# Kernel optimization log

Hardware: AMD Instinct MI355X
Metric: run time of the kernel (lower is better)

Reference implementation:

```python
import jax, jax.numpy as jnp
import numpy as np

N = 197          # tokens (== token_count)
B = 64           # batch
D = 768          # d_model
NH = 12          # n_head
GH = 2           # global_heads
HR = NH // GH    # head_ratio = 6
DH = 64          # d_head
QK = GH * DH     # qk_dim = 128
ML = 3           # mask_levels
EPS = 1e-5


def setup_inputs() -> dict:
    key = jax.random.key(0)
    ks = jax.random.split(key, 9)
    s = 1.0 / np.sqrt(D)
    return {
        "h": jax.random.normal(ks[0], (N, B, D), dtype=jnp.float32),
        "masks": jax.random.uniform(ks[1], (N, N, ML), dtype=jnp.float32),
        "Wq": jax.random.normal(ks[2], (QK, D), dtype=jnp.float32) * s,
        "Wk": jax.random.normal(ks[3], (QK, D), dtype=jnp.float32) * s,
        "Wv": jax.random.normal(ks[4], (NH * DH, D), dtype=jnp.float32) * s,
        "Wo": jax.random.normal(ks[5], (D, NH * DH), dtype=jnp.float32) * s,
        "mask_proj": jnp.ones((ML, NH), dtype=jnp.float32),
        "ln_gamma": jnp.ones((D,), dtype=jnp.float32),
        "ln_beta": jnp.zeros((D,), dtype=jnp.float32),
    }


def reference(h, masks, Wq, Wk, Wv, Wo, mask_proj, ln_gamma, ln_beta):
    scale = 1.0 / np.sqrt(DH)
    # projections (seq-first layout [N, B, ...])
    q = (h @ Wq.T).reshape(N, B, GH, DH)
    k = (h @ Wk.T).reshape(N, B, GH, DH)
    v = (h @ Wv.T).reshape(N, B, NH, DH)
    # global-head scores: [B, GH, i, j]
    score = jnp.einsum('ibgd,jbgd->bgij', q, k) * scale
    # learned mask mix: [i, j, NH] -> [GH, i, j, HR] (g-major head split, matches torch reshape)
    mw = jnp.einsum('ijl,ln->ijn', masks, mask_proj)
    mw = mw.reshape(N, N, GH, HR).transpose(2, 0, 1, 3)
    # broadcast each global head to HR local heads: [B, GH, i, j, HR]
    attn = score[..., None] * mw[None]
    attn = attn.transpose(0, 1, 4, 2, 3).reshape(B, NH, N, N)  # head = g*HR + r
    prob = jax.nn.softmax(attn, axis=-1)
    # AV: [i, B, NH, DH] -> [N, B, NH*DH]
    vec = jnp.einsum('bnij,jbnd->ibnd', prob, v).reshape(N, B, NH * DH)
    out = vec @ Wo.T
    # post-LN residual
    x = h + out
    mu = jnp.mean(x, axis=-1, keepdims=True)
    var = jnp.var(x, axis=-1, keepdims=True)
    return ln_gamma * (x - mu) / jnp.sqrt(var + EPS) + ln_beta
```

## Files before the change

### kernel.cpp

```cpp
#include <hip/hip_runtime.h>
#include <hip/hip_bf16.h>
#include <stdint.h>

#define NTOK 197
#define NPAD 224
#define BATCH 64
#define DMODEL 768
#define NHEAD 12
#define GHEAD 2
#define HRATIO 6
#define DHEAD 64
#define QKDIM 128
#define LNEPS 1e-5f
#define MROWS (NTOK * BATCH)
#define MPAD 12672
#define NKC 24
#define NBAND 99

using f32x4 = __attribute__((ext_vector_type(4))) float;
using s16x8 = __attribute__((ext_vector_type(8))) short;
using s16x4 = __attribute__((ext_vector_type(4))) short;

__device__ __forceinline__ short f2bf(float f) {
  unsigned int x = __float_as_uint(f);
  return (short)((x + 0x7fffu + ((x >> 16) & 1u)) >> 16);
}

__device__ __forceinline__ float bf2f(short s) {
  return __uint_as_float((unsigned)(unsigned short)s << 16);
}

__device__ __forceinline__ void gld16(void* lds, const void* g) {
  __builtin_amdgcn_global_load_lds(
      (const __attribute__((address_space(1))) unsigned int*)g,
      (__attribute__((address_space(3))) unsigned int*)lds, 16, 0, 0);
}

#define NBH (NBAND * NKC)
#define NBQ (8 * NKC)
#define NBW (6 * NKC)
__global__ __launch_bounds__(256)
void prep_kernel(const float* __restrict__ h, const float* __restrict__ Wq,
                 const float* __restrict__ Wk, const float* __restrict__ Wv,
                 const float* __restrict__ Wo, short* __restrict__ hf,
                 short* __restrict__ Wqkvf, short* __restrict__ Wof) {
  const int bb = blockIdx.x, t = threadIdx.x;
  int band, kc, which;
  if (bb < NBH) { which = 0; band = bb / NKC; kc = bb - band * NKC; }
  else if (bb < NBH + NBQ) { int i = bb - NBH; which = 1; band = i / NKC; kc = i - band * NKC; }
  else { int i = bb - NBH - NBQ; which = 2; band = i / NKC; kc = i - band * NKC; }
  short* dstS = (which == 0 ? hf : which == 1 ? Wqkvf : Wof) +
                ((size_t)(band * NKC + kc) * 8) * 512;
#pragma unroll
  for (int uu = 0; uu < 2; ++uu) {
    int u = t + uu * 256;
    int frag = u >> 6, l = u & 63;
    int rl = frag * 16 + (l & 15);
    int k0 = kc * 32 + ((l >> 4) & 3) * 8;
    float4 a = {0, 0, 0, 0}, c = {0, 0, 0, 0};
    if (which == 0) {
      int row = band * 128 + rl;
      if (row < MROWS) {
        const float* p = h + (size_t)row * DMODEL + k0;
        a = *(const float4*)p; c = *(const float4*)(p + 4);
      }
    } else if (which == 1) {
      int row = band * 128 + rl;
      const float* src = (row < 128) ? Wq + (size_t)row * DMODEL
                       : (row < 256) ? Wk + (size_t)(row - 128) * DMODEL
                                     : Wv + (size_t)(row - 256) * DMODEL;
      a = *(const float4*)(src + k0); c = *(const float4*)(src + k0 + 4);
    } else {
      const float* p = Wo + (size_t)(band * 128 + rl) * DMODEL + k0;
      a = *(const float4*)p; c = *(const float4*)(p + 4);
    }
    s16x8 o;
    o[0] = f2bf(a.x); o[1] = f2bf(a.y); o[2] = f2bf(a.z); o[3] = f2bf(a.w);
    o[4] = f2bf(c.x); o[5] = f2bf(c.y); o[6] = f2bf(c.z); o[7] = f2bf(c.w);
    *(s16x8*)(dstS + (size_t)u * 8) = o;
  }
}

__global__ __launch_bounds__(256)
void gemm_frag_kernel(const short* __restrict__ Af, const short* __restrict__ Bf,
                      short* __restrict__ Cout, int M, int NC) {
  const int tid = threadIdx.x;
  const int nwg = gridDim.x * gridDim.y;
  const int orig = blockIdx.y * gridDim.x + blockIdx.x;
  const int qq = nwg >> 3, rr = nwg & 7;
  const int xcd = orig & 7, sidx = orig >> 3;
  const int wg = (xcd < rr ? xcd * (qq + 1) : rr * (qq + 1) + (xcd - rr) * qq) + sidx;
  const int cb = wg % gridDim.x;
  const int rb = wg / gridDim.x;

  const int w = tid >> 6, l = tid & 63;
  const int wr = w >> 1, wc = w & 1;
  const int lm = l & 15, lh = l >> 4;

  const short* pa = Af + ((size_t)(rb * NKC) * 8 + wr * 4) * 512 + l * 8;
  const short* pb = Bf + ((size_t)(cb * NKC) * 8 + wc * 4) * 512 + l * 8;

  f32x4 acc[4][4] = {};
  s16x8 A0[4], B0[4], A1[4], B1[4];

#define LOADF(Ar, Br, kc)                                   \
  do {                                                      \
    const short* qa = pa + (size_t)(kc) * 4096;             \
    const short* qb = pb + (size_t)(kc) * 4096;             \
    Ar[0] = *(const s16x8*)(qa);                            \
    Ar[1] = *(const s16x8*)(qa + 512);                      \
    Ar[2] = *(const s16x8*)(qa + 1024);                     \
    Ar[3] = *(const s16x8*)(qa + 1536);                     \
    Br[0] = *(const s16x8*)(qb);                            \
    Br[1] = *(const s16x8*)(qb + 512);                      \
    Br[2] = *(const s16x8*)(qb + 1024);                     \
    Br[3] = *(const s16x8*)(qb + 1536);                     \
  } while (0)

#define MM(Ar, Br)                                                             \
  do {                                                                         \
    _Pragma("unroll") for (int m = 0; m < 4; ++m)                              \
      _Pragma("unroll") for (int n = 0; n < 4; ++n)                            \
        acc[m][n] = __builtin_amdgcn_mfma_f32_16x16x32_bf16(Ar[m], Br[n],      \
                                                            acc[m][n], 0, 0, 0);\
  } while (0)

  LOADF(A0, B0, 0);
#pragma unroll
  for (int kc = 0; kc < NKC; kc += 2) {
    LOADF(A1, B1, kc + 1);
    MM(A0, B0);
    if (kc + 2 < NKC) LOADF(A0, B0, kc + 2);
    MM(A1, B1);
  }
#undef LOADF
#undef MM

#pragma unroll
  for (int m = 0; m < 4; ++m) {
#pragma unroll
    for (int r = 0; r < 4; ++r) {
      int row = rb * 128 + wr * 64 + m * 16 + lh * 4 + r;
      if (row < M) {
#pragma unroll
        for (int n = 0; n < 4; ++n) {
          int col = cb * 128 + wc * 64 + n * 16 + lm;
          Cout[(size_t)row * NC + col] = f2bf(acc[m][n][r]);
        }
      }
    }
  }
}

__global__ __launch_bounds__(256)
void packall_kernel(const short* __restrict__ Cb, const float* __restrict__ masks,
                    const float* __restrict__ mproj, short* __restrict__ qp,
                    short* __restrict__ kp, short* __restrict__ vT,
                    float* __restrict__ mwp) {
  __shared__ short Vs[NPAD][DHEAD + 1];
  const int bb = blockIdx.x, t = threadIdx.x;
  if (bb < 256) {
    int b = bb >> 2, g = (bb >> 1) & 1, which = bb & 1;
    short* dst = (which ? kp : qp) + ((size_t)b * GHEAD + g) * NPAD * 64;
    int d = t & 63, iofs = t >> 6;
    for (int i0 = 0; i0 < NPAD; i0 += 4) {
      int i = i0 + iofs;
      short v = 0;
      if (i < NTOK)
        v = Cb[(size_t)(i * BATCH + b) * 1024 + which * QKDIM + g * DHEAD + d];
      int dd = which ? ((((d >> 3) ^ (i & 7)) << 3) | (d & 7)) : d;
      dst[i * 64 + dd] = v;
    }
  } else if (bb < 1024) {
    int vv = bb - 256;
    int b = vv / 12, n = vv - b * 12;
    int d = t & 63, iofs = t >> 6;
    for (int i0 = 0; i0 < NPAD; i0 += 4) {
      int i = i0 + iofs;
      short v = 0;
      if (i < NTOK)
        v = Cb[(size_t)(i * BATCH + b) * 1024 + 256 + n * DHEAD + d];
      Vs[i][d] = v;
    }
    __syncthreads();
    short* dst = vT + ((size_t)b * NHEAD + n) * DHEAD * NPAD;
    int sub = t & 63, dr = t >> 6;
    for (int d0 = 0; d0 < DHEAD; d0 += 4) {
      if (sub < 56) {
        int dd = d0 + dr, j0 = sub * 4;
        s16x4 o;
        o[0] = Vs[j0][dd]; o[1] = Vs[j0 + 1][dd];
        o[2] = Vs[j0 + 2][dd]; o[3] = Vs[j0 + 3][dd];
        *(s16x4*)(dst + dd * NPAD + j0) = o;
      }
    }
  } else {
    int e = (bb - 1024) * 256 + t;
    int n = e >> 12;
    int rem = e & 4095;
    int i = rem >> 4, lm = rem & 15;
    float p0 = mproj[n], p1 = mproj[NHEAD + n], p2 = mproj[2 * NHEAD + n];
    float vals[16];
#pragma unroll
    for (int jf = 0; jf < 16; ++jf) vals[jf] = 0.f;
    if (i < NTOK) {
#pragma unroll
      for (int jf = 0; jf < 14; ++jf) {
        int col = jf * 16 + lm;
        if (col < NTOK) {
          const float* mp = masks + ((size_t)i * NTOK + col) * 3;
          vals[jf] = 0.125f * (mp[0] * p0 + mp[1] * p1 + mp[2] * p2);
        }
      }
    }
    float* dst = mwp + (size_t)e * 16;
#pragma unroll
    for (int q = 0; q < 4; ++q) {
      float4 o = make_float4(vals[q * 4], vals[q * 4 + 1], vals[q * 4 + 2], vals[q * 4 + 3]);
      *(float4*)(dst + q * 4) = o;
    }
  }
}

__global__ __launch_bounds__(256, 2)
void attn_fused_kernel(const short* __restrict__ qp, const short* __restrict__ kp,
                       const short* __restrict__ vT, const float* __restrict__ mwp,
                       short* __restrict__ vec_f) {
  const int it = blockIdx.x, b = blockIdx.y, g = blockIdx.z;
  __shared__ short Ks[NPAD * 64];
  __shared__ short Pt[64 * 256];
  __shared__ float rsb[64];
  const int t = threadIdx.x, w = t >> 6, l = t & 63;
  const int lm = l & 15, lh = l >> 4, l7 = l & 7;

  const short* qg = qp + ((size_t)b * GHEAD + g) * NPAD * 64;
  const short* kg = kp + ((size_t)b * GHEAD + g) * NPAD * 64;

#pragma unroll
  for (int s = 0; s < 7; ++s)
    gld16(Ks + s * 2048 + t * 8, kg + s * 2048 + t * 8);
  int qrow = it * 64 + w * 16 + lm;
  if (qrow > NPAD - 1) qrow = NPAD - 1;
  s16x8 a0 = *(const s16x8*)(qg + qrow * 64 + lh * 8);
  s16x8 a1 = *(const s16x8*)(qg + qrow * 64 + 32 + lh * 8);
  __syncthreads();

  f32x4 acc[14] = {};
#pragma unroll
  for (int jf = 0; jf < 14; ++jf) {
    s16x8 kf0 = *(const s16x8*)((const char*)Ks + (jf * 16 + lm) * 128 + ((lh ^ l7) << 4));
    s16x8 kf1 = *(const s16x8*)((const char*)Ks + (jf * 16 + lm) * 128 + (((4 + lh) ^ l7) << 4));
    acc[jf] = __builtin_amdgcn_mfma_f32_16x16x32_bf16(a0, kf0, acc[jf], 0, 0, 0);
    acc[jf] = __builtin_amdgcn_mfma_f32_16x16x32_bf16(a1, kf1, acc[jf], 0, 0, 0);
  }

  const int b4 = b >> 4;
  const int lofs = ((((w & 1) << 1) + (lm >> 3)) * 16 + (b & 15)) * 8 + (lm & 7);

  for (int hh = 0; hh < HRATIO; ++hh) {
    const int n = g * HRATIO + hh;
    const short* vg = vT + ((size_t)b * NHEAD + n) * 64 * NPAD;
    s16x8 vf[7];
#pragma unroll
    for (int ks = 0; ks < 7; ++ks)
      vf[ks] = *(const s16x8*)(vg + (w * 16 + lm) * NPAD + ks * 32 + lh * 8);

#pragma unroll
    for (int r = 0; r < 4; ++r) {
      const int row = w * 16 + lh * 4 + r;
      const int i = it * 64 + row;
      const float* mr = mwp + (((size_t)n * 256 + i) * 16 + lm) * 16;
      f32x4 mv0 = *(const f32x4*)(mr);
      f32x4 mv1 = *(const f32x4*)(mr + 4);
      f32x4 mv2 = *(const f32x4*)(mr + 8);
      f32x4 mv3 = *(const f32x4*)(mr + 12);
      float sum = 0.f;
#pragma unroll
      for (int jf = 0; jf < 13; ++jf) {
        float mwv = (jf < 4) ? mv0[jf] : (jf < 8) ? mv1[jf - 4]
                  : (jf < 12) ? mv2[jf - 8] : mv3[jf - 12];
        float pe = __expf(acc[jf][r] * mwv);
        if (jf == 12 && lm >= 5) pe = 0.f;
        sum += pe;
        int byteoff = row * 512 + (((2 * jf + (lm >> 3)) ^ (row & 7)) << 4) + (lm & 7) * 2;
        *(short*)((char*)Pt + byteoff) = f2bf(pe);
      }
      {
        int byteoff = row * 512 + (((26 + (lm >> 3)) ^ (row & 7)) << 4) + (lm & 7) * 2;
        *(short*)((char*)Pt + byteoff) = 0;
      }
#pragma unroll
      for (int off = 8; off; off >>= 1) sum += __shfl_xor(sum, off);
      if (lm == 0) rsb[row] = 1.f / sum;
    }
    __syncthreads();

    __builtin_amdgcn_s_setprio(1);
    f32x4 oacc[4] = {};
#pragma unroll
    for (int fi = 0; fi < 4; ++fi)
#pragma unroll
      for (int ks = 0; ks < 7; ++ks) {
        s16x8 pa = *(const s16x8*)((const char*)Pt + (fi * 16 + lm) * 512 +
                                   (((ks * 4 + lh) ^ l7) << 4));
        oacc[fi] = __builtin_amdgcn_mfma_f32_16x16x32_bf16(pa, vf[ks], oacc[fi], 0, 0, 0);
      }
    __builtin_amdgcn_s_setprio(0);
    const int kcH = n * 2 + (w >> 1);
#pragma unroll
    for (int fi = 0; fi < 4; ++fi)
#pragma unroll
      for (int r = 0; r < 4; ++r) {
        int ia = it * 64 + fi * 16 + lh * 4 + r;
        if (ia < NTOK) {
          float rsv = rsb[fi * 16 + lh * 4 + r];
          int fragidx = ((it * 32 + fi * 8 + lh * 2 + (r >> 1)) * NKC + kcH) * 8 +
                        ((r & 1) << 2) + b4;
          vec_f[(size_t)fragidx * 512 + lofs] = f2bf(oacc[fi][r] * rsv);
        }
      }
    __syncthreads();
  }
}

__global__ __launch_bounds__(256)
void ln_kernel(const float* __restrict__ h, const short* __restrict__ proj_b,
               float* __restrict__ out, const float* __restrict__ gamma,
               const float* __restrict__ beta) {
  const int m = blockIdx.x;
  const float* hrow = h + (size_t)m * DMODEL;
  const short* prow = proj_b + (size_t)m * DMODEL;
  float* orow = out + (size_t)m * DMODEL;
  const int tid = threadIdx.x;
  float v0 = hrow[tid] + bf2f(prow[tid]);
  float v1 = hrow[tid + 256] + bf2f(prow[tid + 256]);
  float v2 = hrow[tid + 512] + bf2f(prow[tid + 512]);
  float s = v0 + v1 + v2;
  float sq = v0 * v0 + v1 * v1 + v2 * v2;
#pragma unroll
  for (int off = 32; off; off >>= 1) {
    s += __shfl_xor(s, off);
    sq += __shfl_xor(sq, off);
  }
  __shared__ float ss[4], ssq[4];
  const int w = tid >> 6, lane = tid & 63;
  if (lane == 0) { ss[w] = s; ssq[w] = sq; }
  __syncthreads();
  s = ss[0] + ss[1] + ss[2] + ss[3];
  sq = ssq[0] + ssq[1] + ssq[2] + ssq[3];
  const float inv = 1.0f / (float)DMODEL;
  float mu = s * inv;
  float var = sq * inv - mu * mu;
  float rstd = rsqrtf(var + LNEPS);
  orow[tid] = gamma[tid] * (v0 - mu) * rstd + beta[tid];
  orow[tid + 256] = gamma[tid + 256] * (v1 - mu) * rstd + beta[tid + 256];
  orow[tid + 512] = gamma[tid + 512] * (v2 - mu) * rstd + beta[tid + 512];
}

extern "C" void kernel_launch(void* const* d_in, const int* in_sizes, int n_in,
                              void* d_out, int out_size, void* d_ws, size_t ws_size,
                              hipStream_t stream) {
  const float* h     = (const float*)d_in[0];
  const float* masks = (const float*)d_in[1];
  const float* Wq    = (const float*)d_in[2];
  const float* Wk    = (const float*)d_in[3];
  const float* Wv    = (const float*)d_in[4];
  const float* Wo    = (const float*)d_in[5];
  const float* mproj = (const float*)d_in[6];
  const float* gamma = (const float*)d_in[7];
  const float* beta  = (const float*)d_in[8];
  float* out = (float*)d_out;

  char* ws = (char*)d_ws;
  size_t o = 0;
  auto alloc = [&](size_t bytes) { size_t r = o; o += (bytes + 255) & ~(size_t)255; return r; };
  short* hf    = (short*)(ws + alloc((size_t)MPAD * DMODEL * 2));
  short* Cb    = (short*)(ws + alloc((size_t)MPAD * 1024 * 2));
  short* Wqkvf = (short*)(ws + alloc((size_t)1024 * DMODEL * 2));
  short* Wof   = (short*)(ws + alloc((size_t)DMODEL * DMODEL * 2));
  short* qp    = (short*)(ws + alloc((size_t)BATCH * GHEAD * NPAD * DHEAD * 2));
  short* kp    = (short*)(ws + alloc((size_t)BATCH * GHEAD * NPAD * DHEAD * 2));
  short* vT    = (short*)(ws + alloc((size_t)BATCH * NHEAD * DHEAD * NPAD * 2));
  float* mwp   = (float*)(ws + alloc((size_t)NHEAD * 256 * 16 * 16 * 4));
  short* vec_f = hf;
  short* proj_b = Cb;

  prep_kernel<<<NBH + NBQ + NBW, 256, 0, stream>>>(h, Wq, Wk, Wv, Wo, hf, Wqkvf, Wof);
  gemm_frag_kernel<<<dim3(8, NBAND), 256, 0, stream>>>(hf, Wqkvf, Cb, MROWS, 1024);
  packall_kernel<<<1216, 256, 0, stream>>>(Cb, masks, mproj, qp, kp, vT, mwp);
  attn_fused_kernel<<<dim3(4, BATCH, GHEAD), 256, 0, stream>>>(qp, kp, vT, mwp, vec_f);
  gemm_frag_kernel<<<dim3(6, NBAND), 256, 0, stream>>>(vec_f, Wof, proj_b, MROWS, DMODEL);
  ln_kernel<<<MROWS, 256, 0, stream>>>(h, proj_b, out, gamma, beta);
}
```

Baseline: 144.1 us.

## Split attention heads across more blocks, share LDS, write row-major output

The attention kernel now launches 1024 blocks, each handling three of the six local heads, with an XCD-aware block index mapping. K and P tiles share a single LDS buffer so four blocks fit per CU. Attention output is written in plain row-major bf16 instead of the pre-swizzled fragment layout, and the output-projection GEMM gains a template mode that reads A fragments directly from row-major memory. This raises occupancy and parallelism in attention, but the QK^T product is now computed twice per (b, g, it), and the GEMM's A loads become strided.

```diff
diff --git a/kernel.cpp b/kernel.cpp
--- a/kernel.cpp
+++ b/kernel.cpp
@@ -81,6 +81,7 @@
   }
 }
 
+template<int AM>
 __global__ __launch_bounds__(256)
 void gemm_frag_kernel(const short* __restrict__ Af, const short* __restrict__ Bf,
                       short* __restrict__ Cout, int M, int NC) {
@@ -98,23 +99,32 @@
   const int lm = l & 15, lh = l >> 4;
 
   const short* pa = Af + ((size_t)(rb * NKC) * 8 + wr * 4) * 512 + l * 8;
+  const short* paR = Af + (size_t)(rb * 128 + wr * 64 + lm) * DMODEL + lh * 8;
   const short* pb = Bf + ((size_t)(cb * NKC) * 8 + wc * 4) * 512 + l * 8;
 
   f32x4 acc[4][4] = {};
   s16x8 A0[4], B0[4], A1[4], B1[4];
 
-#define LOADF(Ar, Br, kc)                                   \
-  do {                                                      \
-    const short* qa = pa + (size_t)(kc) * 4096;             \
-    const short* qb = pb + (size_t)(kc) * 4096;             \
-    Ar[0] = *(const s16x8*)(qa);                            \
-    Ar[1] = *(const s16x8*)(qa + 512);                      \
-    Ar[2] = *(const s16x8*)(qa + 1024);                     \
-    Ar[3] = *(const s16x8*)(qa + 1536);                     \
-    Br[0] = *(const s16x8*)(qb);                            \
-    Br[1] = *(const s16x8*)(qb + 512);                      \
-    Br[2] = *(const s16x8*)(qb + 1024);                     \
-    Br[3] = *(const s16x8*)(qb + 1536);                     \
+#define LOADF(Ar, Br, kc)                                       \
+  do {                                                          \
+    if (AM == 0) {                                              \
+      const short* qa = pa + (size_t)(kc) * 4096;               \
+      Ar[0] = *(const s16x8*)(qa);                              \
+      Ar[1] = *(const s16x8*)(qa + 512);                        \
+      Ar[2] = *(const s16x8*)(qa + 1024);                       \
+      Ar[3] = *(const s16x8*)(qa + 1536);                       \
+    } else {                                                    \
+      const short* qa = paR + (kc) * 32;                        \
+      Ar[0] = *(const s16x8*)(qa);                              \
+      Ar[1] = *(const s16x8*)(qa + 16 * DMODEL);                \
+      Ar[2] = *(const s16x8*)(qa + 32 * DMODEL);                \
+      Ar[3] = *(const s16x8*)(qa + 48 * DMODEL);                \
+    }                                                           \
+    const short* qb = pb + (size_t)(kc) * 4096;                 \
+    Br[0] = *(const s16x8*)(qb);                                \
+    Br[1] = *(const s16x8*)(qb + 512);                          \
+    Br[2] = *(const s16x8*)(qb + 1024);                         \
+    Br[3] = *(const s16x8*)(qb + 1536);                         \
   } while (0)
 
 #define MM(Ar, Br)                                                             \
@@ -222,13 +232,20 @@
   }
 }
 
-__global__ __launch_bounds__(256, 2)
+__global__ __launch_bounds__(256, 4)
 void attn_fused_kernel(const short* __restrict__ qp, const short* __restrict__ kp,
                        const short* __restrict__ vT, const float* __restrict__ mwp,
-                       short* __restrict__ vec_f) {
-  const int it = blockIdx.x, b = blockIdx.y, g = blockIdx.z;
-  __shared__ short Ks[NPAD * 64];
-  __shared__ short Pt[64 * 256];
+                       short* __restrict__ vec_b) {
+  const int bid = blockIdx.x;
+  const int idx = bid >> 3;
+  const int combo = ((bid & 7) << 1) + (idx >> 6);
+  const int b = idx & 63;
+  const int it = combo & 3;
+  const int gh = combo >> 2;
+  const int g = gh >> 1;
+  const int h0 = g * HRATIO + (gh & 1) * 3;
+
+  __shared__ short U[16384];
   __shared__ float rsb[64];
   const int t = threadIdx.x, w = t >> 6, l = t & 63;
   const int lm = l & 15, lh = l >> 4, l7 = l & 7;
@@ -238,7 +255,7 @@
 
 #pragma unroll
   for (int s = 0; s < 7; ++s)
-    gld16(Ks + s * 2048 + t * 8, kg + s * 2048 + t * 8);
+    gld16(U + s * 2048 + t * 8, kg + s * 2048 + t * 8);
   int qrow = it * 64 + w * 16 + lm;
   if (qrow > NPAD - 1) qrow = NPAD - 1;
   s16x8 a0 = *(const s16x8*)(qg + qrow * 64 + lh * 8);
@@ -248,17 +265,15 @@
   f32x4 acc[14] = {};
 #pragma unroll
   for (int jf = 0; jf < 14; ++jf) {
-    s16x8 kf0 = *(const s16x8*)((const char*)Ks + (jf * 16 + lm) * 128 + ((lh ^ l7) << 4));
-    s16x8 kf1 = *(const s16x8*)((const char*)Ks + (jf * 16 + lm) * 128 + (((4 + lh) ^ l7) << 4));
+    s16x8 kf0 = *(const s16x8*)((const char*)U + (jf * 16 + lm) * 128 + ((lh ^ l7) << 4));
+    s16x8 kf1 = *(const s16x8*)((const char*)U + (jf * 16 + lm) * 128 + (((4 + lh) ^ l7) << 4));
     acc[jf] = __builtin_amdgcn_mfma_f32_16x16x32_bf16(a0, kf0, acc[jf], 0, 0, 0);
     acc[jf] = __builtin_amdgcn_mfma_f32_16x16x32_bf16(a1, kf1, acc[jf], 0, 0, 0);
   }
-
-  const int b4 = b >> 4;
-  const int lofs = ((((w & 1) << 1) + (lm >> 3)) * 16 + (b & 15)) * 8 + (lm & 7);
-
-  for (int hh = 0; hh < HRATIO; ++hh) {
-    const int n = g * HRATIO + hh;
+  __syncthreads();
+
+  for (int hh = 0; hh < 3; ++hh) {
+    const int n = h0 + hh;
     const short* vg = vT + ((size_t)b * NHEAD + n) * 64 * NPAD;
     s16x8 vf[7];
 #pragma unroll
@@ -283,11 +298,11 @@
         if (jf == 12 && lm >= 5) pe = 0.f;
         sum += pe;
         int byteoff = row * 512 + (((2 * jf + (lm >> 3)) ^ (row & 7)) << 4) + (lm & 7) * 2;
-        *(short*)((char*)Pt + byteoff) = f2bf(pe);
+        *(short*)((char*)U + byteoff) = f2bf(pe);
       }
       {
         int byteoff = row * 512 + (((26 + (lm >> 3)) ^ (row & 7)) << 4) + (lm & 7) * 2;
-        *(short*)((char*)Pt + byteoff) = 0;
+        *(short*)((char*)U + byteoff) = 0;
       }
 #pragma unroll
       for (int off = 8; off; off >>= 1) sum += __shfl_xor(sum, off);
@@ -301,12 +316,11 @@
     for (int fi = 0; fi < 4; ++fi)
 #pragma unroll
       for (int ks = 0; ks < 7; ++ks) {
-        s16x8 pa = *(const s16x8*)((const char*)Pt + (fi * 16 + lm) * 512 +
+        s16x8 pa = *(const s16x8*)((const char*)U + (fi * 16 + lm) * 512 +
                                    (((ks * 4 + lh) ^ l7) << 4));
         oacc[fi] = __builtin_amdgcn_mfma_f32_16x16x32_bf16(pa, vf[ks], oacc[fi], 0, 0, 0);
       }
     __builtin_amdgcn_s_setprio(0);
-    const int kcH = n * 2 + (w >> 1);
 #pragma unroll
     for (int fi = 0; fi < 4; ++fi)
 #pragma unroll
@@ -314,9 +328,8 @@
         int ia = it * 64 + fi * 16 + lh * 4 + r;
         if (ia < NTOK) {
           float rsv = rsb[fi * 16 + lh * 4 + r];
-          int fragidx = ((it * 32 + fi * 8 + lh * 2 + (r >> 1)) * NKC + kcH) * 8 +
-                        ((r & 1) << 2) + b4;
-          vec_f[(size_t)fragidx * 512 + lofs] = f2bf(oacc[fi][r] * rsv);
+          vec_b[((size_t)ia * BATCH + b) * DMODEL + n * 64 + w * 16 + lm] =
+              f2bf(oacc[fi][r] * rsv);
         }
       }
     __syncthreads();
@@ -382,13 +395,13 @@
   short* kp    = (short*)(ws + alloc((size_t)BATCH * GHEAD * NPAD * DHEAD * 2));
   short* vT    = (short*)(ws + alloc((size_t)BATCH * NHEAD * DHEAD * NPAD * 2));
   float* mwp   = (float*)(ws + alloc((size_t)NHEAD * 256 * 16 * 16 * 4));
-  short* vec_f = hf;
+  short* vec_b = hf;
   short* proj_b = Cb;
 
   prep_kernel<<<NBH + NBQ + NBW, 256, 0, stream>>>(h, Wq, Wk, Wv, Wo, hf, Wqkvf, Wof);
-  gemm_frag_kernel<<<dim3(8, NBAND), 256, 0, stream>>>(hf, Wqkvf, Cb, MROWS, 1024);
+  gemm_frag_kernel<0><<<dim3(8, NBAND), 256, 0, stream>>>(hf, Wqkvf, Cb, MROWS, 1024);
   packall_kernel<<<1216, 256, 0, stream>>>(Cb, masks, mproj, qp, kp, vT, mwp);
-  attn_fused_kernel<<<dim3(4, BATCH, GHEAD), 256, 0, stream>>>(qp, kp, vT, mwp, vec_f);
-  gemm_frag_kernel<<<dim3(6, NBAND), 256, 0, stream>>>(vec_f, Wof, proj_b, MROWS, DMODEL);
+  attn_fused_kernel<<<1024, 256, 0, stream>>>(qp, kp, vT, mwp, vec_b);
+  gemm_frag_kernel<1><<<dim3(6, NBAND), 256, 0, stream>>>(vec_b, Wof, proj_b, MROWS, DMODEL);
   ln_kernel<<<MROWS, 256, 0, stream>>>(h, proj_b, out, gamma, beta);
 }
```

New measurement: 217.3 us. +50.7%, slower.
